# Optimization experiments

Hardware: AMD Instinct MI355X
Metric: run time of the kernel (lower is better)

The kernel has to match this reference:

```python
import jax, jax.numpy as jnp
import numpy as np

EMBED_DIM = 512
NUM_HEADS = 8
HEAD_DIM = EMBED_DIM // NUM_HEADS
LN_EPS = 1e-5


def setup_inputs() -> dict:
    key = jax.random.key(0)
    ks = jax.random.split(key, 7)
    B, S, E = 2, 4096, EMBED_DIM
    s = 1.0 / np.sqrt(E)
    return {
        "x": jax.random.normal(ks[0], (B, S, E), dtype=jnp.float32),
        "qkv_w": jax.random.normal(ks[1], (E, 3 * E), dtype=jnp.float32) * s,
        "qkv_b": jax.random.normal(ks[2], (3 * E,), dtype=jnp.float32) * 0.01,
        "out_w": jax.random.normal(ks[3], (E, E), dtype=jnp.float32) * s,
        "out_b": jax.random.normal(ks[4], (E,), dtype=jnp.float32) * 0.01,
        "ln_g": jnp.ones((E,), dtype=jnp.float32),
        "ln_b": jnp.zeros((E,), dtype=jnp.float32),
    }


def reference(x, qkv_w, qkv_b, out_w, out_b, ln_g, ln_b):
    B, S, E = x.shape
    H, D = NUM_HEADS, HEAD_DIM
    scale = D ** -0.5
    qkv = x @ qkv_w + qkv_b                     # (B, S, 3E)
    qkv = qkv.reshape(B, S, 3, H, D)
    q, k, v = qkv[:, :, 0], qkv[:, :, 1], qkv[:, :, 2]  # (B, S, H, D)
    scores = jnp.einsum("bshd,bthd->bhst", q, k) * scale  # (B, H, S, S)
    probs = jax.nn.softmax(scores, axis=-1)
    ctx = jnp.einsum("bhst,bthd->bshd", probs, v).reshape(B, S, E)
    out = ctx @ out_w + out_b + x               # residual
    mu = out.mean(-1, keepdims=True)
    var = out.var(-1, keepdims=True)
    return (out - mu) * jax.lax.rsqrt(var + LN_EPS) * ln_g + ln_b
```

## Files before the change

### kernel.cpp

```cpp
#include <hip/hip_runtime.h>
#include <stdint.h>

typedef __bf16 bf16x8 __attribute__((ext_vector_type(8)));
typedef float f32x4 __attribute__((ext_vector_type(4)));
typedef float f32x16 __attribute__((ext_vector_type(16)));
typedef float float4v __attribute__((ext_vector_type(4)));
typedef unsigned short u16x4 __attribute__((ext_vector_type(4)));
typedef unsigned short u16x8 __attribute__((ext_vector_type(8)));
typedef unsigned int u32x4v __attribute__((ext_vector_type(4)));

#define DEVI __device__ __forceinline__

static constexpr int Bv = 2, Sv = 4096, Ev = 512, Hv = 8, Dv = 64;
static constexpr int Mv = Bv * Sv;
static constexpr int N3v = 3 * Ev;
static constexpr float QSCALE = 0.125f * 1.4426950408889634f;
static constexpr float C0 = -8.0f;

#if __has_builtin(__builtin_amdgcn_exp2f)
#define EXP2F(x) __builtin_amdgcn_exp2f(x)
#else
#define EXP2F(x) exp2f(x)
#endif

DEVI unsigned short f2bf(float f) {
    unsigned int u = __builtin_bit_cast(unsigned int, f);
    u += 0x7fffu + ((u >> 16) & 1u);
    return (unsigned short)(u >> 16);
}

DEVI float b2f(unsigned short u) {
    return __builtin_bit_cast(float, (unsigned int)u << 16);
}

DEVI unsigned int cvtpk(float lo, float hi) {
    unsigned int r;
    asm("v_cvt_pk_bf16_f32 %0, %1, %2" : "=v"(r) : "v"(lo), "v"(hi));
    return r;
}

DEVI void gload16(const void* src, void* lds) {
    __builtin_amdgcn_global_load_lds(
        (const __attribute__((address_space(1))) unsigned int*)src,
        (__attribute__((address_space(3))) unsigned int*)lds,
        16, 0, 0);
}

__global__ __launch_bounds__(256) void k_convert(const float* __restrict__ in,
                                                 unsigned short* __restrict__ out, int n4) {
    int i = blockIdx.x * 256 + threadIdx.x;
    int stride = gridDim.x * 256;
    for (; i < n4; i += stride) {
        float4v v = ((const float4v*)in)[i];
        u16x4 o;
        o[0] = f2bf(v[0]); o[1] = f2bf(v[1]); o[2] = f2bf(v[2]); o[3] = f2bf(v[3]);
        ((u16x4*)out)[i] = o;
    }
}

__global__ __launch_bounds__(256) void k_tconv(const float* __restrict__ in,
                                               unsigned short* __restrict__ out, int K, int N) {
    __shared__ float lds[32][36];
    int tilesN = N >> 5;
    int tn = blockIdx.x % tilesN, tk = blockIdx.x / tilesN;
    int k0 = tk << 5, n0 = tn << 5;
    int t = threadIdx.x;
    int r = t >> 3, c4 = (t & 7) << 2;
    float4v v = *(const float4v*)(in + (size_t)(k0 + r) * N + n0 + c4);
    *(float4v*)&lds[r][c4] = v;
    __syncthreads();
    int nn = t >> 3, kc = (t & 7) << 2;
    u16x4 o;
#pragma unroll
    for (int j = 0; j < 4; ++j) o[j] = f2bf(lds[kc + j][nn]);
    *(u16x4*)(out + (size_t)(n0 + nn) * K + k0 + kc) = o;
}

template <int EPI>
__global__ __launch_bounds__(256) void k_gemm(
    const unsigned short* __restrict__ A, const unsigned short* __restrict__ Bt,
    int M, int N, int K, const float* __restrict__ bias,
    unsigned short* __restrict__ Qb, unsigned short* __restrict__ Kb,
    unsigned short* __restrict__ Vtb,
    const float* __restrict__ xres, float* __restrict__ outf) {
    __shared__ char smem[32768];
    char* As = smem;
    char* Bs = smem + 16384;
    int nbt = N >> 7;
    int mb = blockIdx.x / nbt, nbi = blockIdx.x % nbt;
    int m0 = mb << 7, n0 = nbi << 7;
    int tid = threadIdx.x, lane = tid & 63, wave = tid >> 6;
    int wr = wave >> 1, wc = wave & 1;

    f32x4 acc[4][4];
    f32x4 zero = {0.f, 0.f, 0.f, 0.f};
#pragma unroll
    for (int a = 0; a < 4; ++a)
#pragma unroll
        for (int b = 0; b < 4; ++b) acc[a][b] = zero;

    for (int kt = 0; kt < K; kt += 64) {
        __syncthreads();
#pragma unroll
        for (int j = 0; j < 4; ++j) {
            int la = (((wave << 2) + j) << 10) + lane * 16;
            int r = la >> 7, cb = la & 127;
            int cbs = cb ^ ((r & 7) << 4);
            gload16((const char*)(A + (size_t)(m0 + r) * K + kt) + cbs,
                    As + (((wave << 2) + j) << 10));
            gload16((const char*)(Bt + (size_t)(n0 + r) * K + kt) + cbs,
                    Bs + (((wave << 2) + j) << 10));
        }
        asm volatile("s_waitcnt vmcnt(0)" ::: "memory");
        __syncthreads();

        bf16x8 af[4][2], bfr[4][2];
#pragma unroll
        for (int rf = 0; rf < 4; ++rf)
#pragma unroll
            for (int c = 0; c < 2; ++c) {
                int row = (wr << 6) + (rf << 4) + (lane & 15);
                int col = (c << 6) + ((lane >> 4) << 4);
                af[rf][c] = *(const bf16x8*)(As + row * 128 + (col ^ ((row & 7) << 4)));
                int rowb = (wc << 6) + (rf << 4) + (lane & 15);
                bfr[rf][c] = *(const bf16x8*)(Bs + rowb * 128 + (col ^ ((rowb & 7) << 4)));
            }
#pragma unroll
        for (int rf = 0; rf < 4; ++rf)
#pragma unroll
            for (int nf = 0; nf < 4; ++nf)
#pragma unroll
                for (int c = 0; c < 2; ++c)
                    acc[rf][nf] = __builtin_amdgcn_mfma_f32_16x16x32_bf16(
                        af[rf][c], bfr[nf][c], acc[rf][nf], 0, 0, 0);
    }

#pragma unroll
    for (int rf = 0; rf < 4; ++rf)
#pragma unroll
        for (int nf = 0; nf < 4; ++nf) {
            int row0 = m0 + (wr << 6) + (rf << 4) + ((lane >> 4) << 2);
            int col = n0 + (wc << 6) + (nf << 4) + (lane & 15);
            float bv = bias[col];
            if (EPI == 0) {
                int reg = col >> 9, hd = col & 511;
                int h = hd >> 6, d = hd & 63;
                int b = row0 >> 12, s0 = row0 & 4095;
                if (reg == 2) {
                    u16x4 o4;
#pragma unroll
                    for (int i = 0; i < 4; ++i) o4[i] = f2bf(acc[rf][nf][i] + bv);
                    *(u16x4*)(Vtb + ((size_t)((b << 3) + h) * 64 + d) * 4096 + s0) = o4;
                } else {
#pragma unroll
                    for (int i = 0; i < 4; ++i) {
                        float v = acc[rf][nf][i] + bv;
                        size_t idx = ((size_t)((b << 3) + h) * Sv + s0 + i) * Dv + d;
                        if (reg == 0) Qb[idx] = f2bf(v * QSCALE);
                        else          Kb[idx] = f2bf(v);
                    }
                }
            } else {
#pragma unroll
                for (int i = 0; i < 4; ++i) {
                    int row = row0 + i;
                    float v = acc[rf][nf][i] + bv + xres[(size_t)row * N + col];
                    outf[(size_t)row * N + col] = v;
                }
            }
        }
}

__global__ __launch_bounds__(256) void k_attn(const unsigned short* __restrict__ Qb,
                                              const unsigned short* __restrict__ Kb,
                                              const unsigned short* __restrict__ Vtb,
                                              unsigned short* __restrict__ po,
                                              float* __restrict__ pl) {
    __shared__ char smem[32768];
    int bid = blockIdx.x;
    int wg = ((bid & 7) << 6) + (bid >> 3);
    int half = wg & 1, qblk = (wg >> 1) & 15, bh = wg >> 5;
    int tid = threadIdx.x, lane = tid & 63, wave = tid >> 6;
    int l31 = lane & 31, hh = lane >> 5;
    int qbase = (qblk << 8) + (wave << 6);
    int kvbase = half << 11;

    const unsigned short* Kbase = Kb + (size_t)bh * Sv * Dv + (size_t)kvbase * Dv;
    const unsigned short* Vtbase = Vtb + (size_t)bh * Dv * Sv + kvbase;

    bf16x8 qf[2][4];
#pragma unroll
    for (int qs = 0; qs < 2; ++qs)
#pragma unroll
        for (int tp = 0; tp < 4; ++tp)
            qf[qs][tp] = *(const bf16x8*)(Qb + ((size_t)bh * Sv + qbase + (qs << 5) + l31) * Dv +
                                          (tp << 4) + (hh << 3));

    const char* src[4];
    int strd[4];
    int ldsoff[4];
#pragma unroll
    for (int j = 0; j < 4; ++j) {
        int off = ((wave << 2) + j) << 10;
        int loff = off + lane * 16;
        ldsoff[j] = off;
        if (off < 8192) {
            int r = loff >> 7, cb = loff & 127;
            src[j] = (const char*)(Kbase + (size_t)r * Dv) + (cb ^ ((r & 7) << 4));
            strd[j] = 64 * Dv * 2;
        } else {
            int lo2 = loff - 8192;
            int r = lo2 >> 7, cb = lo2 & 127;
            src[j] = (const char*)(Vtbase + (size_t)r * Sv) + (cb ^ ((r & 7) << 4));
            strd[j] = 64 * 2;
        }
    }

    int koff[2][4], voff[2][2][2];
#pragma unroll
    for (int c = 0; c < 2; ++c) {
        int krow = (c << 5) + l31;
        int ksw = (krow & 7) << 4;
#pragma unroll
        for (int tp = 0; tp < 4; ++tp)
            koff[c][tp] = krow * 128 + (((tp << 5) + (hh << 4)) ^ ksw);
#pragma unroll
        for (int tl = 0; tl < 2; ++tl) {
            int vcb = (c << 6) + (tl << 5) + (hh << 4);
#pragma unroll
            for (int dt = 0; dt < 2; ++dt) {
                int vrow = (dt << 5) + l31;
                voff[c][tl][dt] = vrow * 128 + (vcb ^ ((vrow & 7) << 4));
            }
        }
    }

    f32x16 o[2][2];
#pragma unroll
    for (int qs = 0; qs < 2; ++qs)
#pragma unroll
        for (int dt = 0; dt < 2; ++dt)
#pragma unroll
            for (int r = 0; r < 16; ++r) o[qs][dt][r] = 0.f;
    float lsum[2] = {0.f, 0.f};

#pragma unroll
    for (int j = 0; j < 4; ++j) gload16(src[j], smem + ldsoff[j]);
    __syncthreads();

    for (int kt = 0; kt < 32; ++kt) {
        if (kt < 31) {
            int nb = (kt + 1) & 1;
#pragma unroll
            for (int j = 0; j < 4; ++j)
                gload16(src[j] + (size_t)(kt + 1) * strd[j], smem + nb * 16384 + ldsoff[j]);
        }
        char* Ks = smem + (kt & 1) * 16384;
        char* Vs = Ks + 8192;

#pragma unroll
        for (int c = 0; c < 2; ++c) {
            bf16x8 kf[4];
#pragma unroll
            for (int tp = 0; tp < 4; ++tp)
                kf[tp] = *(const bf16x8*)(Ks + koff[c][tp]);
            bf16x8 vf[2][2];
#pragma unroll
            for (int tl = 0; tl < 2; ++tl)
#pragma unroll
                for (int dt = 0; dt < 2; ++dt)
                    vf[tl][dt] = *(const bf16x8*)(Vs + voff[c][tl][dt]);

#pragma unroll
            for (int qs = 0; qs < 2; ++qs) {
                f32x16 sc;
#pragma unroll
                for (int r = 0; r < 16; ++r) sc[r] = C0;
                __builtin_amdgcn_s_setprio(1);
#pragma unroll
                for (int tp = 0; tp < 4; ++tp)
                    sc = __builtin_amdgcn_mfma_f32_32x32x16_bf16(kf[tp], qf[qs][tp], sc, 0, 0, 0);
                __builtin_amdgcn_s_setprio(0);

#pragma unroll
                for (int r = 0; r < 16; ++r) sc[r] = EXP2F(sc[r]);
                float s0 = (sc[0] + sc[1]) + (sc[2] + sc[3]);
                float s1 = (sc[4] + sc[5]) + (sc[6] + sc[7]);
                float s2 = (sc[8] + sc[9]) + (sc[10] + sc[11]);
                float s3 = (sc[12] + sc[13]) + (sc[14] + sc[15]);
                lsum[qs] += (s0 + s1) + (s2 + s3);

                unsigned int W[8];
#pragma unroll
                for (int i = 0; i < 8; ++i) W[i] = cvtpk(sc[2 * i], sc[2 * i + 1]);

#pragma unroll
                for (int tl = 0; tl < 2; ++tl) {
                    unsigned int a1 = W[4 * tl], b1 = W[4 * tl + 2];
                    unsigned int a2 = W[4 * tl + 1], b2 = W[4 * tl + 3];
                    asm volatile("v_permlane32_swap_b32 %0, %1" : "+v"(a1), "+v"(b1));
                    asm volatile("v_permlane32_swap_b32 %0, %1" : "+v"(a2), "+v"(b2));
                    u32x4v uu;
                    uu[0] = a1; uu[1] = a2; uu[2] = b1; uu[3] = b2;
                    bf16x8 pf = __builtin_bit_cast(bf16x8, uu);
                    __builtin_amdgcn_s_setprio(1);
#pragma unroll
                    for (int dt = 0; dt < 2; ++dt)
                        o[qs][dt] = __builtin_amdgcn_mfma_f32_32x32x16_bf16(vf[tl][dt], pf,
                                                                            o[qs][dt], 0, 0, 0);
                    __builtin_amdgcn_s_setprio(0);
                }
            }
        }
        __syncthreads();
    }

#pragma unroll
    for (int qs = 0; qs < 2; ++qs) {
        float ls = lsum[qs] + __shfl_xor(lsum[qs], 32, 64);
        int qrow = qbase + (qs << 5) + l31;
        if (!hh) pl[((size_t)half * 16 + bh) * Sv + qrow] = ls;
        size_t obase = (((size_t)half * 16 + bh) * Sv + qrow) * 64;
#pragma unroll
        for (int dt = 0; dt < 2; ++dt)
#pragma unroll
            for (int rp = 0; rp < 8; ++rp) {
                int r = rp << 1;
                int d = (dt << 5) + (r & 3) + ((r >> 2) << 3) + (hh << 2);
                unsigned int w = cvtpk(o[qs][dt][r], o[qs][dt][r + 1]);
                *(unsigned int*)(po + obase + d) = w;
            }
    }
}

__global__ __launch_bounds__(256) void k_merge(const unsigned short* __restrict__ po,
                                               const float* __restrict__ pl,
                                               unsigned short* __restrict__ ctx) {
    int t = blockIdx.x * 256 + threadIdx.x;
    int d8 = t & 7, s = (t >> 3) & 4095, bh = t >> 15;
    int b = bh >> 3, h = bh & 7;
    size_t r0 = ((size_t)bh * 4096 + s) * 64 + (d8 << 3);
    size_t r1 = r0 + (size_t)16 * 4096 * 64;
    u16x8 pa = *(const u16x8*)(po + r0);
    u16x8 pb = *(const u16x8*)(po + r1);
    float inv = 1.f / (pl[(size_t)bh * 4096 + s] + pl[(size_t)16 * 4096 + bh * 4096 + s]);
    u32x4v w;
#pragma unroll
    for (int j = 0; j < 4; ++j) {
        float lo = (b2f(pa[2 * j]) + b2f(pb[2 * j])) * inv;
        float hi = (b2f(pa[2 * j + 1]) + b2f(pb[2 * j + 1])) * inv;
        w[j] = cvtpk(lo, hi);
    }
    *(u32x4v*)(ctx + ((size_t)b * 4096 + s) * 512 + (h << 6) + (d8 << 3)) = w;
}

__global__ __launch_bounds__(256) void k_ln(const float* __restrict__ in,
                                            const float* __restrict__ g,
                                            const float* __restrict__ bta,
                                            float* __restrict__ out) {
    int wave = threadIdx.x >> 6, lane = threadIdx.x & 63;
    size_t row = (size_t)blockIdx.x * 4 + wave;
    const float* p = in + row * 512 + lane * 8;
    float4v v0 = *(const float4v*)p;
    float4v v1 = *(const float4v*)(p + 4);
    float s = 0.f, q = 0.f;
#pragma unroll
    for (int j = 0; j < 4; ++j) {
        s += v0[j] + v1[j];
        q += v0[j] * v0[j] + v1[j] * v1[j];
    }
#pragma unroll
    for (int off = 1; off < 64; off <<= 1) {
        s += __shfl_xor(s, off, 64);
        q += __shfl_xor(q, off, 64);
    }
    float mu = s * (1.f / 512.f);
    float var = q * (1.f / 512.f) - mu * mu;
    float rs = rsqrtf(var + 1e-5f);
    int c = lane * 8;
    float4v o0, o1;
#pragma unroll
    for (int j = 0; j < 4; ++j) {
        o0[j] = (v0[j] - mu) * rs * g[c + j] + bta[c + j];
        o1[j] = (v1[j] - mu) * rs * g[c + 4 + j] + bta[c + 4 + j];
    }
    *(float4v*)(out + row * 512 + c) = o0;
    *(float4v*)(out + row * 512 + c + 4) = o1;
}

extern "C" void kernel_launch(void* const* d_in, const int* in_sizes, int n_in,
                              void* d_out, int out_size, void* d_ws, size_t ws_size,
                              hipStream_t stream) {
    const float* x     = (const float*)d_in[0];
    const float* qkv_w = (const float*)d_in[1];
    const float* qkv_b = (const float*)d_in[2];
    const float* out_w = (const float*)d_in[3];
    const float* out_b = (const float*)d_in[4];
    const float* ln_g  = (const float*)d_in[5];
    const float* ln_b  = (const float*)d_in[6];
    float* out = (float*)d_out;
    char* ws = (char*)d_ws;

    unsigned short* xb    = (unsigned short*)(ws);
    unsigned short* wqkvT = (unsigned short*)(ws + 8388608);
    unsigned short* owT   = (unsigned short*)(ws + 9961472);
    unsigned short* Qb    = (unsigned short*)(ws + 10485760);
    unsigned short* Kb    = (unsigned short*)(ws + 18874368);
    unsigned short* Vtb   = (unsigned short*)(ws + 27262976);
    unsigned short* ctxb  = (unsigned short*)(ws + 35651584);
    unsigned short* po    = (unsigned short*)(ws + 44040192);
    float* tmp            = (float*)(ws + 44040192);
    float* pl             = (float*)(ws + 60817408);

    k_convert<<<2048, 256, 0, stream>>>(x, xb, Mv * Ev / 4);
    k_tconv<<<(512 / 32) * (1536 / 32), 256, 0, stream>>>(qkv_w, wqkvT, 512, 1536);
    k_tconv<<<(512 / 32) * (512 / 32), 256, 0, stream>>>(out_w, owT, 512, 512);
    k_gemm<0><<<(Mv / 128) * (N3v / 128), 256, 0, stream>>>(
        xb, wqkvT, Mv, N3v, Ev, qkv_b, Qb, Kb, Vtb, nullptr, nullptr);
    k_attn<<<512, 256, 0, stream>>>(Qb, Kb, Vtb, po, pl);
    k_merge<<<2048, 256, 0, stream>>>(po, pl, ctxb);
    k_gemm<1><<<(Mv / 128) * (Ev / 128), 256, 0, stream>>>(
        ctxb, owT, Mv, Ev, Ev, out_b, nullptr, nullptr, nullptr, x, tmp);
    k_ln<<<Mv / 4, 256, 0, stream>>>(tmp, ln_g, ln_b, out);
}
```

Baseline: 174.6 us.

## Give each wave private K/V buffers to remove block-wide barriers

Each wave now loads its own copy of the K and V tiles into a private 16KB double-buffered LDS region, in 32-key chunks. This replaces the shared 64-key tiles that needed __syncthreads every iteration, and ordering now relies on per-wave s_waitcnt vmcnt. The cost is four times more global/L2 traffic for K/V, since all waves reload the same data, and doubled LDS use (64KB). It also sets launch_bounds to 2 blocks per CU. The V layout changes to 64-byte rows with a different swizzle.

Measured after the change: 158.0 us. 1.1x faster.

```diff
diff --git a/kernel.cpp b/kernel.cpp
--- a/kernel.cpp
+++ b/kernel.cpp
@@ -171,12 +171,17 @@
         }
 }
 
-__global__ __launch_bounds__(256) void k_attn(const unsigned short* __restrict__ Qb,
-                                              const unsigned short* __restrict__ Kb,
-                                              const unsigned short* __restrict__ Vtb,
-                                              unsigned short* __restrict__ po,
-                                              float* __restrict__ pl) {
-    __shared__ char smem[32768];
+struct AttnCtx {
+    const char* Ks;
+    const char* Vs;
+};
+
+__global__ __launch_bounds__(256, 2) void k_attn(const unsigned short* __restrict__ Qb,
+                                                 const unsigned short* __restrict__ Kb,
+                                                 const unsigned short* __restrict__ Vtb,
+                                                 unsigned short* __restrict__ po,
+                                                 float* __restrict__ pl) {
+    __shared__ char smem[65536];
     int bid = blockIdx.x;
     int wg = ((bid & 7) << 6) + (bid >> 3);
     int half = wg & 1, qblk = (wg >> 1) & 15, bh = wg >> 5;
@@ -185,8 +190,9 @@
     int qbase = (qblk << 8) + (wave << 6);
     int kvbase = half << 11;
 
-    const unsigned short* Kbase = Kb + (size_t)bh * Sv * Dv + (size_t)kvbase * Dv;
-    const unsigned short* Vtbase = Vtb + (size_t)bh * Dv * Sv + kvbase;
+    const char* Kbase = (const char*)(Kb + (size_t)bh * Sv * Dv + (size_t)kvbase * Dv);
+    const char* Vtbase = (const char*)(Vtb + (size_t)bh * Dv * Sv + kvbase);
+    char* mybuf = smem + wave * 16384;
 
     bf16x8 qf[2][4];
 #pragma unroll
@@ -196,44 +202,34 @@
             qf[qs][tp] = *(const bf16x8*)(Qb + ((size_t)bh * Sv + qbase + (qs << 5) + l31) * Dv +
                                           (tp << 4) + (hh << 3));
 
-    const char* src[4];
-    int strd[4];
-    int ldsoff[4];
+    const char* srck[4];
+    const char* srcv[4];
 #pragma unroll
     for (int j = 0; j < 4; ++j) {
-        int off = ((wave << 2) + j) << 10;
-        int loff = off + lane * 16;
-        ldsoff[j] = off;
-        if (off < 8192) {
+        {
+            int loff = (j << 10) + lane * 16;
             int r = loff >> 7, cb = loff & 127;
-            src[j] = (const char*)(Kbase + (size_t)r * Dv) + (cb ^ ((r & 7) << 4));
-            strd[j] = 64 * Dv * 2;
-        } else {
-            int lo2 = loff - 8192;
-            int r = lo2 >> 7, cb = lo2 & 127;
-            src[j] = (const char*)(Vtbase + (size_t)r * Sv) + (cb ^ ((r & 7) << 4));
-            strd[j] = 64 * 2;
-        }
-    }
-
-    int koff[2][4], voff[2][2][2];
-#pragma unroll
-    for (int c = 0; c < 2; ++c) {
-        int krow = (c << 5) + l31;
-        int ksw = (krow & 7) << 4;
-#pragma unroll
-        for (int tp = 0; tp < 4; ++tp)
-            koff[c][tp] = krow * 128 + (((tp << 5) + (hh << 4)) ^ ksw);
-#pragma unroll
-        for (int tl = 0; tl < 2; ++tl) {
-            int vcb = (c << 6) + (tl << 5) + (hh << 4);
-#pragma unroll
-            for (int dt = 0; dt < 2; ++dt) {
-                int vrow = (dt << 5) + l31;
-                voff[c][tl][dt] = vrow * 128 + (vcb ^ ((vrow & 7) << 4));
-            }
-        }
-    }
+            srck[j] = Kbase + (size_t)r * 128 + (cb ^ ((r & 7) << 4));
+        }
+        {
+            int loff = (j << 10) + lane * 16;
+            int r = loff >> 6, cb = loff & 63;
+            srcv[j] = Vtbase + (size_t)r * 8192 + (cb ^ ((r & 6) << 3));
+        }
+    }
+
+    int koff[4], voff[4];
+#pragma unroll
+    for (int tp = 0; tp < 4; ++tp)
+        koff[tp] = l31 * 128 + (((tp << 5) + (hh << 4)) ^ ((l31 & 7) << 4));
+#pragma unroll
+    for (int tl = 0; tl < 2; ++tl)
+#pragma unroll
+        for (int dt = 0; dt < 2; ++dt) {
+            int row = (dt << 5) + l31;
+            int col = (tl << 5) + (hh << 4);
+            voff[tl * 2 + dt] = row * 64 + (col ^ ((row & 6) << 3));
+        }
 
     f32x16 o[2][2];
 #pragma unroll
@@ -245,75 +241,68 @@
     float lsum[2] = {0.f, 0.f};
 
 #pragma unroll
-    for (int j = 0; j < 4; ++j) gload16(src[j], smem + ldsoff[j]);
-    __syncthreads();
-
-    for (int kt = 0; kt < 32; ++kt) {
-        if (kt < 31) {
-            int nb = (kt + 1) & 1;
-#pragma unroll
-            for (int j = 0; j < 4; ++j)
-                gload16(src[j] + (size_t)(kt + 1) * strd[j], smem + nb * 16384 + ldsoff[j]);
-        }
-        char* Ks = smem + (kt & 1) * 16384;
-        char* Vs = Ks + 8192;
-
-#pragma unroll
-        for (int c = 0; c < 2; ++c) {
-            bf16x8 kf[4];
-#pragma unroll
-            for (int tp = 0; tp < 4; ++tp)
-                kf[tp] = *(const bf16x8*)(Ks + koff[c][tp]);
-            bf16x8 vf[2][2];
-#pragma unroll
-            for (int tl = 0; tl < 2; ++tl)
-#pragma unroll
-                for (int dt = 0; dt < 2; ++dt)
-                    vf[tl][dt] = *(const bf16x8*)(Vs + voff[c][tl][dt]);
-
-#pragma unroll
-            for (int qs = 0; qs < 2; ++qs) {
-                f32x16 sc;
-#pragma unroll
-                for (int r = 0; r < 16; ++r) sc[r] = C0;
-                __builtin_amdgcn_s_setprio(1);
-#pragma unroll
-                for (int tp = 0; tp < 4; ++tp)
-                    sc = __builtin_amdgcn_mfma_f32_32x32x16_bf16(kf[tp], qf[qs][tp], sc, 0, 0, 0);
-                __builtin_amdgcn_s_setprio(0);
-
-#pragma unroll
-                for (int r = 0; r < 16; ++r) sc[r] = EXP2F(sc[r]);
-                float s0 = (sc[0] + sc[1]) + (sc[2] + sc[3]);
-                float s1 = (sc[4] + sc[5]) + (sc[6] + sc[7]);
-                float s2 = (sc[8] + sc[9]) + (sc[10] + sc[11]);
-                float s3 = (sc[12] + sc[13]) + (sc[14] + sc[15]);
-                lsum[qs] += (s0 + s1) + (s2 + s3);
-
-                unsigned int W[8];
-#pragma unroll
-                for (int i = 0; i < 8; ++i) W[i] = cvtpk(sc[2 * i], sc[2 * i + 1]);
-
-#pragma unroll
-                for (int tl = 0; tl < 2; ++tl) {
-                    unsigned int a1 = W[4 * tl], b1 = W[4 * tl + 2];
-                    unsigned int a2 = W[4 * tl + 1], b2 = W[4 * tl + 3];
-                    asm volatile("v_permlane32_swap_b32 %0, %1" : "+v"(a1), "+v"(b1));
-                    asm volatile("v_permlane32_swap_b32 %0, %1" : "+v"(a2), "+v"(b2));
-                    u32x4v uu;
-                    uu[0] = a1; uu[1] = a2; uu[2] = b1; uu[3] = b2;
-                    bf16x8 pf = __builtin_bit_cast(bf16x8, uu);
-                    __builtin_amdgcn_s_setprio(1);
-#pragma unroll
-                    for (int dt = 0; dt < 2; ++dt)
-                        o[qs][dt] = __builtin_amdgcn_mfma_f32_32x32x16_bf16(vf[tl][dt], pf,
-                                                                            o[qs][dt], 0, 0, 0);
-                    __builtin_amdgcn_s_setprio(0);
-                }
-            }
-        }
-        __syncthreads();
-    }
+    for (int j = 0; j < 4; ++j) {
+        gload16(srck[j], mybuf + (j << 10));
+        gload16(srcv[j], mybuf + 4096 + (j << 10));
+    }
+
+#define COMPUTE_CHUNK(KSP, VSP)                                                          \
+    {                                                                                    \
+        bf16x8 kf[4], vf[4];                                                             \
+        _Pragma("unroll") for (int tp = 0; tp < 4; ++tp)                                 \
+            kf[tp] = *(const bf16x8*)((KSP) + koff[tp]);                                 \
+        _Pragma("unroll") for (int i = 0; i < 4; ++i)                                    \
+            vf[i] = *(const bf16x8*)((VSP) + voff[i]);                                   \
+        _Pragma("unroll") for (int qs = 0; qs < 2; ++qs) {                               \
+            f32x16 sc;                                                                   \
+            _Pragma("unroll") for (int r = 0; r < 16; ++r) sc[r] = C0;                   \
+            __builtin_amdgcn_s_setprio(1);                                               \
+            _Pragma("unroll") for (int tp = 0; tp < 4; ++tp)                             \
+                sc = __builtin_amdgcn_mfma_f32_32x32x16_bf16(kf[tp], qf[qs][tp], sc, 0, 0, 0); \
+            __builtin_amdgcn_s_setprio(0);                                               \
+            _Pragma("unroll") for (int r = 0; r < 16; ++r) sc[r] = EXP2F(sc[r]);         \
+            float s0 = (sc[0] + sc[1]) + (sc[2] + sc[3]);                                \
+            float s1 = (sc[4] + sc[5]) + (sc[6] + sc[7]);                                \
+            float s2 = (sc[8] + sc[9]) + (sc[10] + sc[11]);                              \
+            float s3 = (sc[12] + sc[13]) + (sc[14] + sc[15]);                            \
+            lsum[qs] += (s0 + s1) + (s2 + s3);                                           \
+            unsigned int W[8];                                                           \
+            _Pragma("unroll") for (int i = 0; i < 8; ++i)                                \
+                W[i] = cvtpk(sc[2 * i], sc[2 * i + 1]);                                  \
+            _Pragma("unroll") for (int tl = 0; tl < 2; ++tl) {                           \
+                unsigned int a1 = W[4 * tl], b1 = W[4 * tl + 2];                         \
+                unsigned int a2 = W[4 * tl + 1], b2 = W[4 * tl + 3];                     \
+                asm volatile("v_permlane32_swap_b32 %0, %1" : "+v"(a1), "+v"(b1));       \
+                asm volatile("v_permlane32_swap_b32 %0, %1" : "+v"(a2), "+v"(b2));       \
+                u32x4v uu;                                                               \
+                uu[0] = a1; uu[1] = a2; uu[2] = b1; uu[3] = b2;                          \
+                bf16x8 pf = __builtin_bit_cast(bf16x8, uu);                              \
+                __builtin_amdgcn_s_setprio(1);                                           \
+                _Pragma("unroll") for (int dt = 0; dt < 2; ++dt)                         \
+                    o[qs][dt] = __builtin_amdgcn_mfma_f32_32x32x16_bf16(                 \
+                        vf[tl * 2 + dt], pf, o[qs][dt], 0, 0, 0);                        \
+                __builtin_amdgcn_s_setprio(0);                                           \
+            }                                                                            \
+        }                                                                                \
+    }
+
+    for (int kt = 0; kt < 63; ++kt) {
+        char* nbuf = mybuf + (((kt + 1) & 1) << 13);
+#pragma unroll
+        for (int j = 0; j < 4; ++j) {
+            gload16(srck[j] + (size_t)(kt + 1) * 4096, nbuf + (j << 10));
+            gload16(srcv[j] + (size_t)(kt + 1) * 64, nbuf + 4096 + (j << 10));
+        }
+        asm volatile("s_waitcnt vmcnt(8)" ::: "memory");
+        char* cbuf = mybuf + ((kt & 1) << 13);
+        COMPUTE_CHUNK(cbuf, cbuf + 4096);
+    }
+    asm volatile("s_waitcnt vmcnt(0)" ::: "memory");
+    {
+        char* cbuf = mybuf + ((63 & 1) << 13);
+        COMPUTE_CHUNK(cbuf, cbuf + 4096);
+    }
+#undef COMPUTE_CHUNK
 
 #pragma unroll
     for (int qs = 0; qs < 2; ++qs) {
```
